# Performance work log

Measured on AMD Instinct MI355X. Metric: run time of the kernel, lower is better.

## Reference

```python
import jax, jax.numpy as jnp
import numpy as np

C = 1536          # interim_dim
D2 = 2 * C        # 3072, fc_nlb dim
LN_EPS = 1e-5


def setup_inputs() -> dict:
    key = jax.random.key(0)
    ks = jax.random.split(key, 24)
    B, L = 32, 1024
    s = 0.02
    inp = {
        "x": jax.random.normal(ks[0], (B, C), dtype=jnp.float32),
        "lfb_feats": jax.random.normal(ks[1], (B, L, C), dtype=jnp.float32),
        # 1x1 Conv1d weights act as (C_out, C_in) matmuls
        "theta_w": jax.random.normal(ks[2], (C, C), dtype=jnp.float32) * s,
        "theta_b": jnp.zeros((C,), dtype=jnp.float32),
        "phi_w": jax.random.normal(ks[3], (C, C), dtype=jnp.float32) * s,
        "phi_b": jnp.zeros((C,), dtype=jnp.float32),
        "gi_w": jax.random.normal(ks[4], (C, C), dtype=jnp.float32) * s,
        "gi_b": jnp.zeros((C,), dtype=jnp.float32),
        "ln_g": jnp.ones((C,), dtype=jnp.float32),
        "ln_b": jnp.zeros((C,), dtype=jnp.float32),
        "fc_w": jax.random.normal(ks[5], (C, C), dtype=jnp.float32) * s,
        "fc_b": jnp.zeros((C,), dtype=jnp.float32),
        "fc_nlb_w": jax.random.normal(ks[6], (D2, D2), dtype=jnp.float32) * s,
        "fc_nlb_b": jnp.zeros((D2,), dtype=jnp.float32),
        "fc1_w": jax.random.normal(ks[7], (1, 1024), dtype=jnp.float32) * s,
        "fc1_b": jnp.zeros((1,), dtype=jnp.float32),
        "fc2_w": jax.random.normal(ks[8], (1, 1024), dtype=jnp.float32) * s,
        "fc2_b": jnp.zeros((1,), dtype=jnp.float32),
        "fc3_w": jax.random.normal(ks[9], (1, 1024), dtype=jnp.float32) * s,
        "fc3_b": jnp.zeros((1,), dtype=jnp.float32),
        "fct_w": jax.random.normal(ks[10], (1, D2), dtype=jnp.float32) * s,
        "fct_b": jnp.zeros((1,), dtype=jnp.float32),
    }
    return inp


def _layernorm(x, g, b):
    mu = jnp.mean(x, axis=-1, keepdims=True)
    var = jnp.mean(jnp.square(x - mu), axis=-1, keepdims=True)
    return (x - mu) * jax.lax.rsqrt(var + LN_EPS) * g + b


def reference(x, lfb_feats, theta_w, theta_b, phi_w, phi_b, gi_w, gi_b,
              ln_g, ln_b, fc_w, fc_b, fc_nlb_w, fc_nlb_b,
              fc1_w, fc1_b, fc2_w, fc2_b, fc3_w, fc3_b, fct_w, fct_b):
    # --- _NLBlock on feats = x.unsqueeze(1): query sequence length is 1 ---
    # note: scale = 1/sqrt(1/C) = sqrt(C) (as in the original code)
    scale = jnp.sqrt(jnp.asarray(C, dtype=x.dtype))
    theta = x @ theta_w.T + theta_b                       # (B, C)
    phi = lfb_feats @ phi_w.T + phi_b                     # (B, L, C)
    gi = lfb_feats @ gi_w.T + gi_b                        # (B, L, C)
    scores = jnp.einsum('bc,blc->bl', theta, phi) * scale  # (B, L)
    attn = jax.nn.softmax(scores, axis=-1)
    o = jnp.einsum('bl,blc->bc', attn, gi)                # (B, C)
    o = jax.nn.relu(_layernorm(o, ln_g, ln_b))
    o = o @ fc_w.T + fc_b                                 # dropout -> identity (eval)
    longterm = o + x                                      # residual, (B, C)

    # --- head ---
    feats = jnp.concatenate([x, longterm], axis=1)        # (B, 2C)
    feats = jax.nn.relu(feats @ fc_nlb_w.T + fc_nlb_b)    # dropout -> identity
    f1 = feats[:, :1024]
    f2 = feats[:, 1024:2048]
    f3 = feats[:, 2048:3072]
    p1 = f1 @ fc1_w.T + fc1_b
    p2 = f2 @ fc2_w.T + fc2_b
    p3 = f3 @ fc3_w.T + fc3_b
    pt = feats @ fct_w.T + fct_b
    return jnp.concatenate([p1, p2, p3, pt], axis=1)      # (B, 4)
```

## Files before the change

kernel.cpp:

```cpp
#include <hip/hip_runtime.h>
#include <math.h>

#define B 32
#define C 1536
#define D2 3072
#define L 1024
#define KC 64
#define CH 16
#define LPW 16

__device__ inline float dot4(float4 a, float4 b) {
    return a.x * b.x + a.y * b.y + a.z * b.z + a.w * b.w;
}
__device__ inline float4 ld4(const float* p) { return *(const float4*)p; }
__device__ inline void   st4(float* p, float4 v) { *(float4*)p = v; }

__device__ inline int sw(int row, int q) {
    return row * KC + ((q ^ ((row >> 2) & 7)) << 2);
}

__global__ __launch_bounds__(256) void transpose_k(const float* __restrict__ src,
                                                   float* __restrict__ dst, int n) {
    __shared__ float tile[32][33];
    int bx = blockIdx.x * 32, by = blockIdx.y * 32;
    int tx = threadIdx.x & 31, ty0 = threadIdx.x >> 5;
    #pragma unroll
    for (int r = 0; r < 4; ++r) {
        int ty = ty0 + r * 8;
        tile[ty][tx] = src[(size_t)(by + ty) * n + bx + tx];
    }
    __syncthreads();
    #pragma unroll
    for (int r = 0; r < 4; ++r) {
        int ty = ty0 + r * 8;
        dst[(size_t)(bx + ty) * n + by + tx] = tile[tx][ty];
    }
}

__global__ __launch_bounds__(256) void gemm32(const float* __restrict__ A,
                                              const float* __restrict__ W,
                                              float* __restrict__ part,
                                              int N, int K, int kchunks) {
    __shared__ float xs[32 * KC];
    __shared__ float wsm[64 * KC];
    int tid = threadIdx.x;
    int j0 = blockIdx.x * 64;
    int kb = blockIdx.y;
    int tb = tid & 15;
    int tj = tid >> 4;

    float4 acc0 = make_float4(0.f, 0.f, 0.f, 0.f);
    float4 acc1 = make_float4(0.f, 0.f, 0.f, 0.f);

    for (int c = 0; c < kchunks; ++c) {
        int k0 = (kb * kchunks + c) * KC;
        __syncthreads();
        #pragma unroll
        for (int p = 0; p < 2; ++p) {
            int f = tid + 256 * p;
            int row = f >> 4, q = f & 15;
            st4(xs + sw(row, q), ld4(A + (size_t)row * K + k0 + 4 * q));
        }
        #pragma unroll
        for (int p = 0; p < 4; ++p) {
            int f = tid + 256 * p;
            int row = f >> 4, q = f & 15;
            st4(wsm + sw(row, q), ld4(W + (size_t)(j0 + row) * K + k0 + 4 * q));
        }
        __syncthreads();
        #pragma unroll
        for (int kq = 0; kq < 16; ++kq) {
            float4 x0 = ld4(xs + sw(2 * tb, kq));
            float4 x1 = ld4(xs + sw(2 * tb + 1, kq));
            float4 w0 = ld4(wsm + sw(4 * tj + 0, kq));
            float4 w1 = ld4(wsm + sw(4 * tj + 1, kq));
            float4 w2 = ld4(wsm + sw(4 * tj + 2, kq));
            float4 w3 = ld4(wsm + sw(4 * tj + 3, kq));
            acc0.x += dot4(x0, w0); acc0.y += dot4(x0, w1);
            acc0.z += dot4(x0, w2); acc0.w += dot4(x0, w3);
            acc1.x += dot4(x1, w0); acc1.y += dot4(x1, w1);
            acc1.z += dot4(x1, w2); acc1.w += dot4(x1, w3);
        }
    }
    st4(part + ((size_t)kb * 32 + 2 * tb + 0) * N + j0 + 4 * tj, acc0);
    st4(part + ((size_t)kb * 32 + 2 * tb + 1) * N + j0 + 4 * tj, acc1);
}

__global__ __launch_bounds__(256) void reduce_part(const float* __restrict__ part,
                                                   const float* __restrict__ bias,
                                                   const float* __restrict__ addx,
                                                   float* __restrict__ out,
                                                   float* __restrict__ feats,
                                                   int N, int mode) {
    int i = blockIdx.x * 256 + threadIdx.x;
    int b = i / N, j = i % N;
    float s = 0.f;
    #pragma unroll
    for (int kk = 0; kk < 12; ++kk) s += part[((size_t)kk * 32 + b) * N + j];
    if (bias) s += bias[j];
    if (mode == 2) {
        float xv = addx[i];
        feats[(size_t)b * D2 + j] = xv;
        feats[(size_t)b * D2 + C + j] = s + xv;
    } else {
        out[i] = s;
    }
}

__global__ __launch_bounds__(256) void reduce_ln_relu(const float* __restrict__ part,
                                                      const float* __restrict__ bias,
                                                      const float* __restrict__ g,
                                                      const float* __restrict__ bt,
                                                      float* __restrict__ out) {
    int b = blockIdx.x, tid = threadIdx.x;
    __shared__ float r1[4], r2[4];
    float lv[6];
    float s1 = 0.f, s2 = 0.f;
    #pragma unroll
    for (int t = 0; t < 6; ++t) {
        int c = tid + 256 * t;
        float acc = 0.f;
        #pragma unroll
        for (int kk = 0; kk < 12; ++kk) acc += part[((size_t)kk * 32 + b) * C + c];
        acc += bias[c];
        lv[t] = acc; s1 += acc; s2 += acc * acc;
    }
    #pragma unroll
    for (int off = 32; off > 0; off >>= 1) {
        s1 += __shfl_xor(s1, off, 64);
        s2 += __shfl_xor(s2, off, 64);
    }
    int wave = tid >> 6, lane = tid & 63;
    if (lane == 0) { r1[wave] = s1; r2[wave] = s2; }
    __syncthreads();
    s1 = r1[0] + r1[1] + r1[2] + r1[3];
    s2 = r2[0] + r2[1] + r2[2] + r2[3];
    float mu = s1 / (float)C;
    float var = s2 / (float)C - mu * mu;
    float rstd = 1.0f / sqrtf(var + 1e-5f);
    #pragma unroll
    for (int t = 0; t < 6; ++t) {
        int c = tid + 256 * t;
        float y = (lv[t] - mu) * rstd * g[c] + bt[c];
        out[(size_t)b * C + c] = fmaxf(y, 0.f);
    }
}

__global__ __launch_bounds__(256) void flash_k(const float* __restrict__ u,
                                               const float* __restrict__ lfb,
                                               float* __restrict__ pm,
                                               float* __restrict__ ps,
                                               float* __restrict__ pv) {
    int chunk = blockIdx.x;
    int b = blockIdx.y;
    int wave = threadIdx.x >> 6;
    int lane = threadIdx.x & 63;
    int widx = chunk * 4 + wave;

    const float scale = 39.19183588453085f;

    float uu[24];
    const float* ub = u + (size_t)b * C;
    #pragma unroll
    for (int t = 0; t < 6; ++t)
        *(float4*)(uu + 4 * t) = ld4(ub + 4 * lane + 256 * t);

    float m = -INFINITY, s = 0.f;
    float vv[24];
    #pragma unroll
    for (int t = 0; t < 24; ++t) vv[t] = 0.f;

    int l0 = chunk * (L / CH) + wave;
    for (int i = 0; i < LPW; ++i) {
        int l = l0 + i * 4;
        const float* row = lfb + ((size_t)b * L + l) * C;
        float xx[24];
        #pragma unroll
        for (int t = 0; t < 6; ++t)
            *(float4*)(xx + 4 * t) = ld4(row + 4 * lane + 256 * t);
        float d = 0.f;
        #pragma unroll
        for (int t = 0; t < 24; ++t) d += xx[t] * uu[t];
        #pragma unroll
        for (int off = 32; off > 0; off >>= 1) d += __shfl_xor(d, off, 64);
        float score = d * scale;
        float mn = fmaxf(m, score);
        float alpha = __expf(m - mn);
        float p = __expf(score - mn);
        s = s * alpha + p;
        #pragma unroll
        for (int t = 0; t < 24; ++t) vv[t] = vv[t] * alpha + p * xx[t];
        m = mn;
    }

    if (lane == 0) { pm[b * 64 + widx] = m; ps[b * 64 + widx] = s; }
    float* pvb = pv + ((size_t)b * 64 + widx) * C;
    #pragma unroll
    for (int t = 0; t < 6; ++t)
        st4(pvb + 4 * lane + 256 * t, *(float4*)(vv + 4 * t));
}

__global__ __launch_bounds__(256) void combine_k(const float* __restrict__ pm,
                                                 const float* __restrict__ ps,
                                                 const float* __restrict__ pv,
                                                 float* __restrict__ v) {
    int cc = blockIdx.x;
    int b = blockIdx.y;
    int tid = threadIdx.x;
    __shared__ float coef[64];
    if (tid < 64) {
        float mj = pm[b * 64 + tid];
        float M = mj;
        #pragma unroll
        for (int off = 32; off > 0; off >>= 1) M = fmaxf(M, __shfl_xor(M, off, 64));
        float ej = expf(mj - M);
        float S = ps[b * 64 + tid] * ej;
        #pragma unroll
        for (int off = 32; off > 0; off >>= 1) S += __shfl_xor(S, off, 64);
        coef[tid] = ej / S;
    }
    __syncthreads();
    int c = cc * 256 + tid;
    float acc = 0.f;
    #pragma unroll 8
    for (int j = 0; j < 64; ++j)
        acc += coef[j] * pv[((size_t)b * 64 + j) * C + c];
    v[(size_t)b * C + c] = acc;
}

__global__ __launch_bounds__(256) void final_k(const float* __restrict__ partH,
                                               const float* __restrict__ fcn_b,
                                               const float* __restrict__ w1, const float* __restrict__ b1,
                                               const float* __restrict__ w2, const float* __restrict__ b2,
                                               const float* __restrict__ w3, const float* __restrict__ b3,
                                               const float* __restrict__ wt, const float* __restrict__ bt,
                                               float* __restrict__ out) {
    int b = blockIdx.x;
    int tid = threadIdx.x;
    float ph0 = 0.f, ph1 = 0.f, ph2 = 0.f, ptv = 0.f;
    #pragma unroll
    for (int t = 0; t < 12; ++t) {
        int j = tid + 256 * t;
        float s = 0.f;
        #pragma unroll
        for (int ss = 0; ss < 12; ++ss)
            s += partH[((size_t)ss * 32 + b) * D2 + j];
        s += fcn_b[j];
        s = fmaxf(s, 0.f);
        ptv += s * wt[j];
        int jj = tid + 256 * (t & 3);
        if (t < 4)       ph0 += s * w1[jj];
        else if (t < 8)  ph1 += s * w2[jj];
        else             ph2 += s * w3[jj];
    }
    #pragma unroll
    for (int off = 32; off > 0; off >>= 1) {
        ph0 += __shfl_xor(ph0, off, 64);
        ph1 += __shfl_xor(ph1, off, 64);
        ph2 += __shfl_xor(ph2, off, 64);
        ptv += __shfl_xor(ptv, off, 64);
    }
    __shared__ float red[4][4];
    int wave = tid >> 6, lane = tid & 63;
    if (lane == 0) {
        red[wave][0] = ph0; red[wave][1] = ph1; red[wave][2] = ph2; red[wave][3] = ptv;
    }
    __syncthreads();
    if (tid < 4) {
        float v = red[0][tid] + red[1][tid] + red[2][tid] + red[3][tid];
        float bias = (tid == 0) ? b1[0] : (tid == 1) ? b2[0] : (tid == 2) ? b3[0] : bt[0];
        out[b * 4 + tid] = v + bias;
    }
}

extern "C" void kernel_launch(void* const* d_in, const int* in_sizes, int n_in,
                              void* d_out, int out_size, void* d_ws, size_t ws_size,
                              hipStream_t stream) {
    (void)in_sizes; (void)n_in; (void)out_size; (void)ws_size;
    const float* x       = (const float*)d_in[0];
    const float* lfb     = (const float*)d_in[1];
    const float* theta_w = (const float*)d_in[2];
    const float* theta_b = (const float*)d_in[3];
    const float* phi_w   = (const float*)d_in[4];
    const float* gi_w    = (const float*)d_in[6];
    const float* gi_b    = (const float*)d_in[7];
    const float* ln_g    = (const float*)d_in[8];
    const float* ln_b    = (const float*)d_in[9];
    const float* fc_w    = (const float*)d_in[10];
    const float* fc_b    = (const float*)d_in[11];
    const float* fcn_w   = (const float*)d_in[12];
    const float* fcn_b   = (const float*)d_in[13];
    const float* w1 = (const float*)d_in[14]; const float* b1 = (const float*)d_in[15];
    const float* w2 = (const float*)d_in[16]; const float* b2 = (const float*)d_in[17];
    const float* w3 = (const float*)d_in[18]; const float* b3 = (const float*)d_in[19];
    const float* wt = (const float*)d_in[20]; const float* bt = (const float*)d_in[21];
    float* out = (float*)d_out;
    float* w = (float*)d_ws;

    float* phiT  = w;
    float* partT = w + 2359296;
    float* partU = w + 2949120;
    float* partG = w + 3538944;
    float* partF = w + 4128768;
    float* partH = w + 4718592;
    float* pv    = w + 5898240;
    float* pm    = w + 9043968;
    float* ps    = w + 9046016;
    float* theta = w + 9048064;
    float* u     = w + 9097216;
    float* vbuf  = w + 9146368;
    float* oln   = w + 9195520;
    float* feats = w + 9244672;

    transpose_k<<<dim3(48, 48), 256, 0, stream>>>(phi_w, phiT, C);

    gemm32<<<dim3(24, 12), 256, 0, stream>>>(x, theta_w, partT, C, C, 2);
    reduce_part<<<192, 256, 0, stream>>>(partT, theta_b, nullptr, theta, nullptr, C, 0);

    gemm32<<<dim3(24, 12), 256, 0, stream>>>(theta, phiT, partU, C, C, 2);
    reduce_part<<<192, 256, 0, stream>>>(partU, nullptr, nullptr, u, nullptr, C, 0);

    flash_k<<<dim3(CH, B), 256, 0, stream>>>(u, lfb, pm, ps, pv);
    combine_k<<<dim3(6, B), 256, 0, stream>>>(pm, ps, pv, vbuf);

    gemm32<<<dim3(24, 12), 256, 0, stream>>>(vbuf, gi_w, partG, C, C, 2);
    reduce_ln_relu<<<B, 256, 0, stream>>>(partG, gi_b, ln_g, ln_b, oln);

    gemm32<<<dim3(24, 12), 256, 0, stream>>>(oln, fc_w, partF, C, C, 2);
    reduce_part<<<192, 256, 0, stream>>>(partF, fc_b, x, nullptr, feats, C, 2);

    gemm32<<<dim3(48, 12), 256, 0, stream>>>(feats, fcn_w, partH, D2, D2, 4);

    final_k<<<B, 256, 0, stream>>>(partH, fcn_b, w1, b1, w2, b2, w3, b3, wt, bt, out);
}
```

Before: 443.4 us.

## Replace split-K partial buffers and reduce kernels with atomic accumulation

Split-K GEMMs now atomically add their partial results into output buffers that a new init kernel pre-fills with the biases. This removes the separate reduce kernels and their partial-buffer traffic. The phi weight transpose kernel is replaced by a GEMM variant that transposes while loading into shared memory. The feats concat and residual are fused into the final head GEMM's input load. In exchange, results depend on atomic ordering and there is extra atomic traffic.

```diff
diff --git a/kernel.cpp b/kernel.cpp
--- a/kernel.cpp
+++ b/kernel.cpp
@@ -19,27 +19,25 @@
     return row * KC + ((q ^ ((row >> 2) & 7)) << 2);
 }
 
-__global__ __launch_bounds__(256) void transpose_k(const float* __restrict__ src,
-                                                   float* __restrict__ dst, int n) {
-    __shared__ float tile[32][33];
-    int bx = blockIdx.x * 32, by = blockIdx.y * 32;
-    int tx = threadIdx.x & 31, ty0 = threadIdx.x >> 5;
-    #pragma unroll
-    for (int r = 0; r < 4; ++r) {
-        int ty = ty0 + r * 8;
-        tile[ty][tx] = src[(size_t)(by + ty) * n + bx + tx];
-    }
-    __syncthreads();
-    #pragma unroll
-    for (int r = 0; r < 4; ++r) {
-        int ty = ty0 + r * 8;
-        dst[(size_t)(bx + ty) * n + by + tx] = tile[tx][ty];
-    }
+__global__ __launch_bounds__(256) void init_k(float* __restrict__ theta, const float* __restrict__ tb,
+                                              float* __restrict__ u,
+                                              float* __restrict__ obuf, const float* __restrict__ gib,
+                                              float* __restrict__ o2, const float* __restrict__ fcb,
+                                              float* __restrict__ h, const float* __restrict__ fcnb) {
+    int i = blockIdx.x * 256 + threadIdx.x;
+    if (i < 32 * C) {
+        int j = i % C;
+        theta[i] = tb[j];
+        u[i]     = 0.f;
+        obuf[i]  = gib[j];
+        o2[i]    = fcb[j];
+    }
+    if (i < 32 * D2) h[i] = fcnb[i % D2];
 }
 
 __global__ __launch_bounds__(256) void gemm32(const float* __restrict__ A,
                                               const float* __restrict__ W,
-                                              float* __restrict__ part,
+                                              float* __restrict__ out,
                                               int N, int K, int kchunks) {
     __shared__ float xs[32 * KC];
     __shared__ float wsm[64 * KC];
@@ -82,36 +80,139 @@
             acc1.z += dot4(x1, w2); acc1.w += dot4(x1, w3);
         }
     }
-    st4(part + ((size_t)kb * 32 + 2 * tb + 0) * N + j0 + 4 * tj, acc0);
-    st4(part + ((size_t)kb * 32 + 2 * tb + 1) * N + j0 + 4 * tj, acc1);
-}
-
-__global__ __launch_bounds__(256) void reduce_part(const float* __restrict__ part,
-                                                   const float* __restrict__ bias,
-                                                   const float* __restrict__ addx,
-                                                   float* __restrict__ out,
-                                                   float* __restrict__ feats,
-                                                   int N, int mode) {
-    int i = blockIdx.x * 256 + threadIdx.x;
-    int b = i / N, j = i % N;
-    float s = 0.f;
-    #pragma unroll
-    for (int kk = 0; kk < 12; ++kk) s += part[((size_t)kk * 32 + b) * N + j];
-    if (bias) s += bias[j];
-    if (mode == 2) {
-        float xv = addx[i];
-        feats[(size_t)b * D2 + j] = xv;
-        feats[(size_t)b * D2 + C + j] = s + xv;
-    } else {
-        out[i] = s;
-    }
-}
-
-__global__ __launch_bounds__(256) void reduce_ln_relu(const float* __restrict__ part,
-                                                      const float* __restrict__ bias,
-                                                      const float* __restrict__ g,
-                                                      const float* __restrict__ bt,
-                                                      float* __restrict__ out) {
+    float* p0 = out + (size_t)(2 * tb + 0) * N + j0 + 4 * tj;
+    float* p1 = out + (size_t)(2 * tb + 1) * N + j0 + 4 * tj;
+    atomicAdd(p0 + 0, acc0.x); atomicAdd(p0 + 1, acc0.y);
+    atomicAdd(p0 + 2, acc0.z); atomicAdd(p0 + 3, acc0.w);
+    atomicAdd(p1 + 0, acc1.x); atomicAdd(p1 + 1, acc1.y);
+    atomicAdd(p1 + 2, acc1.z); atomicAdd(p1 + 3, acc1.w);
+}
+
+__global__ __launch_bounds__(256) void gemm32_nt(const float* __restrict__ A,
+                                                 const float* __restrict__ W,
+                                                 float* __restrict__ out,
+                                                 int N, int K, int kchunks) {
+    __shared__ float xs[32 * KC];
+    __shared__ float wsm[64 * KC];
+    int tid = threadIdx.x;
+    int j0 = blockIdx.x * 64;
+    int kb = blockIdx.y;
+    int tb = tid & 15;
+    int tj = tid >> 4;
+
+    float4 acc0 = make_float4(0.f, 0.f, 0.f, 0.f);
+    float4 acc1 = make_float4(0.f, 0.f, 0.f, 0.f);
+
+    for (int c = 0; c < kchunks; ++c) {
+        int k0 = (kb * kchunks + c) * KC;
+        __syncthreads();
+        #pragma unroll
+        for (int p = 0; p < 2; ++p) {
+            int f = tid + 256 * p;
+            int row = f >> 4, q = f & 15;
+            st4(xs + sw(row, q), ld4(A + (size_t)row * K + k0 + 4 * q));
+        }
+        #pragma unroll
+        for (int p = 0; p < 4; ++p) {
+            int f = tid + 256 * p;
+            int r = f >> 4;
+            int cq = f & 15;
+            float4 v = ld4(W + (size_t)(k0 + r) * N + j0 + 4 * cq);
+            wsm[sw(4 * cq + 0, r >> 2) + (r & 3)] = v.x;
+            wsm[sw(4 * cq + 1, r >> 2) + (r & 3)] = v.y;
+            wsm[sw(4 * cq + 2, r >> 2) + (r & 3)] = v.z;
+            wsm[sw(4 * cq + 3, r >> 2) + (r & 3)] = v.w;
+        }
+        __syncthreads();
+        #pragma unroll
+        for (int kq = 0; kq < 16; ++kq) {
+            float4 x0 = ld4(xs + sw(2 * tb, kq));
+            float4 x1 = ld4(xs + sw(2 * tb + 1, kq));
+            float4 w0 = ld4(wsm + sw(4 * tj + 0, kq));
+            float4 w1 = ld4(wsm + sw(4 * tj + 1, kq));
+            float4 w2 = ld4(wsm + sw(4 * tj + 2, kq));
+            float4 w3 = ld4(wsm + sw(4 * tj + 3, kq));
+            acc0.x += dot4(x0, w0); acc0.y += dot4(x0, w1);
+            acc0.z += dot4(x0, w2); acc0.w += dot4(x0, w3);
+            acc1.x += dot4(x1, w0); acc1.y += dot4(x1, w1);
+            acc1.z += dot4(x1, w2); acc1.w += dot4(x1, w3);
+        }
+    }
+    float* p0 = out + (size_t)(2 * tb + 0) * N + j0 + 4 * tj;
+    float* p1 = out + (size_t)(2 * tb + 1) * N + j0 + 4 * tj;
+    atomicAdd(p0 + 0, acc0.x); atomicAdd(p0 + 1, acc0.y);
+    atomicAdd(p0 + 2, acc0.z); atomicAdd(p0 + 3, acc0.w);
+    atomicAdd(p1 + 0, acc1.x); atomicAdd(p1 + 1, acc1.y);
+    atomicAdd(p1 + 2, acc1.z); atomicAdd(p1 + 3, acc1.w);
+}
+
+__global__ __launch_bounds__(256) void gemm32_h(const float* __restrict__ x,
+                                                const float* __restrict__ o2,
+                                                const float* __restrict__ W,
+                                                float* __restrict__ out,
+                                                int N, int K, int kchunks) {
+    __shared__ float xs[32 * KC];
+    __shared__ float wsm[64 * KC];
+    int tid = threadIdx.x;
+    int j0 = blockIdx.x * 64;
+    int kb = blockIdx.y;
+    int tb = tid & 15;
+    int tj = tid >> 4;
+
+    float4 acc0 = make_float4(0.f, 0.f, 0.f, 0.f);
+    float4 acc1 = make_float4(0.f, 0.f, 0.f, 0.f);
+
+    for (int c = 0; c < kchunks; ++c) {
+        int k0 = (kb * kchunks + c) * KC;
+        __syncthreads();
+        #pragma unroll
+        for (int p = 0; p < 2; ++p) {
+            int f = tid + 256 * p;
+            int row = f >> 4, q = f & 15;
+            int kk = k0 + 4 * q;
+            float4 v;
+            if (kk < C) {
+                v = ld4(x + (size_t)row * C + kk);
+            } else {
+                float4 a = ld4(x + (size_t)row * C + kk - C);
+                float4 b = ld4(o2 + (size_t)row * C + kk - C);
+                v = make_float4(a.x + b.x, a.y + b.y, a.z + b.z, a.w + b.w);
+            }
+            st4(xs + sw(row, q), v);
+        }
+        #pragma unroll
+        for (int p = 0; p < 4; ++p) {
+            int f = tid + 256 * p;
+            int row = f >> 4, q = f & 15;
+            st4(wsm + sw(row, q), ld4(W + (size_t)(j0 + row) * K + k0 + 4 * q));
+        }
+        __syncthreads();
+        #pragma unroll
+        for (int kq = 0; kq < 16; ++kq) {
+            float4 x0 = ld4(xs + sw(2 * tb, kq));
+            float4 x1 = ld4(xs + sw(2 * tb + 1, kq));
+            float4 w0 = ld4(wsm + sw(4 * tj + 0, kq));
+            float4 w1 = ld4(wsm + sw(4 * tj + 1, kq));
+            float4 w2 = ld4(wsm + sw(4 * tj + 2, kq));
+            float4 w3 = ld4(wsm + sw(4 * tj + 3, kq));
+            acc0.x += dot4(x0, w0); acc0.y += dot4(x0, w1);
+            acc0.z += dot4(x0, w2); acc0.w += dot4(x0, w3);
+            acc1.x += dot4(x1, w0); acc1.y += dot4(x1, w1);
+            acc1.z += dot4(x1, w2); acc1.w += dot4(x1, w3);
+        }
+    }
+    float* p0 = out + (size_t)(2 * tb + 0) * N + j0 + 4 * tj;
+    float* p1 = out + (size_t)(2 * tb + 1) * N + j0 + 4 * tj;
+    atomicAdd(p0 + 0, acc0.x); atomicAdd(p0 + 1, acc0.y);
+    atomicAdd(p0 + 2, acc0.z); atomicAdd(p0 + 3, acc0.w);
+    atomicAdd(p1 + 0, acc1.x); atomicAdd(p1 + 1, acc1.y);
+    atomicAdd(p1 + 2, acc1.z); atomicAdd(p1 + 3, acc1.w);
+}
+
+__global__ __launch_bounds__(256) void ln_relu(const float* __restrict__ obuf,
+                                               const float* __restrict__ g,
+                                               const float* __restrict__ bt,
+                                               float* __restrict__ out) {
     int b = blockIdx.x, tid = threadIdx.x;
     __shared__ float r1[4], r2[4];
     float lv[6];
@@ -119,10 +220,7 @@
     #pragma unroll
     for (int t = 0; t < 6; ++t) {
         int c = tid + 256 * t;
-        float acc = 0.f;
-        #pragma unroll
-        for (int kk = 0; kk < 12; ++kk) acc += part[((size_t)kk * 32 + b) * C + c];
-        acc += bias[c];
+        float acc = obuf[(size_t)b * C + c];
         lv[t] = acc; s1 += acc; s2 += acc * acc;
     }
     #pragma unroll
@@ -228,8 +326,7 @@
     v[(size_t)b * C + c] = acc;
 }
 
-__global__ __launch_bounds__(256) void final_k(const float* __restrict__ partH,
-                                               const float* __restrict__ fcn_b,
+__global__ __launch_bounds__(256) void final_k(const float* __restrict__ h,
                                                const float* __restrict__ w1, const float* __restrict__ b1,
                                                const float* __restrict__ w2, const float* __restrict__ b2,
                                                const float* __restrict__ w3, const float* __restrict__ b3,
@@ -241,12 +338,7 @@
     #pragma unroll
     for (int t = 0; t < 12; ++t) {
         int j = tid + 256 * t;
-        float s = 0.f;
-        #pragma unroll
-        for (int ss = 0; ss < 12; ++ss)
-            s += partH[((size_t)ss * 32 + b) * D2 + j];
-        s += fcn_b[j];
-        s = fmaxf(s, 0.f);
+        float s = fmaxf(h[(size_t)b * D2 + j], 0.f);
         ptv += s * wt[j];
         int jj = tid + 256 * (t & 3);
         if (t < 4)       ph0 += s * w1[jj];
@@ -297,39 +389,32 @@
     float* out = (float*)d_out;
     float* w = (float*)d_ws;
 
-    float* phiT  = w;
-    float* partT = w + 2359296;
-    float* partU = w + 2949120;
-    float* partG = w + 3538944;
-    float* partF = w + 4128768;
-    float* partH = w + 4718592;
-    float* pv    = w + 5898240;
-    float* pm    = w + 9043968;
-    float* ps    = w + 9046016;
-    float* theta = w + 9048064;
-    float* u     = w + 9097216;
-    float* vbuf  = w + 9146368;
-    float* oln   = w + 9195520;
-    float* feats = w + 9244672;
-
-    transpose_k<<<dim3(48, 48), 256, 0, stream>>>(phi_w, phiT, C);
-
-    gemm32<<<dim3(24, 12), 256, 0, stream>>>(x, theta_w, partT, C, C, 2);
-    reduce_part<<<192, 256, 0, stream>>>(partT, theta_b, nullptr, theta, nullptr, C, 0);
-
-    gemm32<<<dim3(24, 12), 256, 0, stream>>>(theta, phiT, partU, C, C, 2);
-    reduce_part<<<192, 256, 0, stream>>>(partU, nullptr, nullptr, u, nullptr, C, 0);
+    float* pv    = w;
+    float* pm    = w + 3145728;
+    float* ps    = w + 3147776;
+    float* theta = w + 3149824;
+    float* u     = w + 3198976;
+    float* vbuf  = w + 3248128;
+    float* obuf  = w + 3297280;
+    float* oln   = w + 3346432;
+    float* o2    = w + 3395584;
+    float* h     = w + 3444736;
+
+    init_k<<<384, 256, 0, stream>>>(theta, theta_b, u, obuf, gi_b, o2, fc_b, h, fcn_b);
+
+    gemm32<<<dim3(24, 12), 256, 0, stream>>>(x, theta_w, theta, C, C, 2);
+
+    gemm32_nt<<<dim3(24, 12), 256, 0, stream>>>(theta, phi_w, u, C, C, 2);
 
     flash_k<<<dim3(CH, B), 256, 0, stream>>>(u, lfb, pm, ps, pv);
     combine_k<<<dim3(6, B), 256, 0, stream>>>(pm, ps, pv, vbuf);
 
-    gemm32<<<dim3(24, 12), 256, 0, stream>>>(vbuf, gi_w, partG, C, C, 2);
-    reduce_ln_relu<<<B, 256, 0, stream>>>(partG, gi_b, ln_g, ln_b, oln);
-
-    gemm32<<<dim3(24, 12), 256, 0, stream>>>(oln, fc_w, partF, C, C, 2);
-    reduce_part<<<192, 256, 0, stream>>>(partF, fc_b, x, nullptr, feats, C, 2);
-
-    gemm32<<<dim3(48, 12), 256, 0, stream>>>(feats, fcn_w, partH, D2, D2, 4);
-
-    final_k<<<B, 256, 0, stream>>>(partH, fcn_b, w1, b1, w2, b2, w3, b3, wt, bt, out);
-}
+    gemm32<<<dim3(24, 12), 256, 0, stream>>>(vbuf, gi_w, obuf, C, C, 2);
+    ln_relu<<<B, 256, 0, stream>>>(obuf, ln_g, ln_b, oln);
+
+    gemm32<<<dim3(24, 12), 256, 0, stream>>>(oln, fc_w, o2, C, C, 2);
+
+    gemm32_h<<<dim3(48, 12), 256, 0, stream>>>(x, o2, fcn_w, h, D2, D2, 4);
+
+    final_k<<<B, 256, 0, stream>>>(h, w1, b1, w2, b2, w3, b3, wt, bt, out);
+}
```

New measurement: 477.7 us. +7.7%, slower.
